# Optimization experiments

Measured on AMD Instinct MI355X. Metric: run time of the kernel, lower is better.

## Reference

```python
import jax, jax.numpy as jnp
import numpy as np

ANG = 7
N = ANG * ANG          # 49 views
CENTER = N // 2        # index 24 = central view
EDGE_C = 150.0
ALPHA = 0.1
CROP = 8
GAUSS = jnp.array([[0.0751, 0.1238, 0.0751],
                   [0.1238, 0.2042, 0.1238],
                   [0.0751, 0.1238, 0.0751]], dtype=jnp.float32)


def _edge_aware_smoothness(D, I):
    # D: [b,h,w] disparity; I: [b,3,h,w] center view
    gx = I[:, :, :, 1:] - I[:, :, :, :-1]
    gy = I[:, :, 1:, :] - I[:, :, :-1, :]
    wx = jnp.exp(-EDGE_C * jnp.mean(jnp.abs(gx), axis=1, keepdims=True))
    wy = jnp.exp(-EDGE_C * jnp.mean(jnp.abs(gy), axis=1, keepdims=True))
    Du = D[:, None]
    dgx = Du[:, :, :, 1:] - Du[:, :, :, :-1]
    dgy = Du[:, :, 1:, :] - Du[:, :, :-1, :]
    lx = jnp.mean((wx * jnp.abs(dgx))[:, :, CROP:-CROP, CROP:-CROP])
    ly = jnp.mean((wy * jnp.abs(dgy))[:, :, CROP:-CROP, CROP:-CROP])
    return (lx + ly) / 2.0


def _warp_all(pred, x):
    # Backward-warp each of the 49 views toward the center view using the
    # per-pixel disparity scaled by the view's angular offset (bilinear,
    # border-clamped) -- standard light-field warping (warp_all in the repo).
    # pred: [b,h,w]; x: [b,3,N,h,w] -> warped [b,3,N,h,w]
    b, c, n, h, w = x.shape
    off = jnp.arange(ANG, dtype=pred.dtype) - (ANG // 2)
    du = jnp.repeat(off, ANG)   # row (u) offset per view, [N]
    dv = jnp.tile(off, ANG)     # col (v) offset per view, [N]
    gy = jnp.arange(h, dtype=pred.dtype)[:, None]
    gx = jnp.arange(w, dtype=pred.dtype)[None, :]
    p = pred[:, None, :, :]                                # [b,1,h,w]
    cy = jnp.clip(gy[None, None] + p * du[None, :, None, None], 0.0, h - 1)
    cx = jnp.clip(gx[None, None] + p * dv[None, :, None, None], 0.0, w - 1)
    y0f = jnp.floor(cy); x0f = jnp.floor(cx)
    ty = (cy - y0f)[..., None]; tx = (cx - x0f)[..., None]
    y0 = y0f.astype(jnp.int32); x0 = x0f.astype(jnp.int32)
    y1 = jnp.minimum(y0 + 1, h - 1); x1 = jnp.minimum(x0 + 1, w - 1)
    img = jnp.transpose(x, (0, 2, 3, 4, 1)).reshape(b, n, h * w, c)

    def gather(yi, xi):
        idx = (yi * w + xi).reshape(b, n, h * w, 1)
        return jnp.take_along_axis(img, idx, axis=2).reshape(b, n, h, w, c)

    out = (gather(y0, x0) * (1 - ty) * (1 - tx)
           + gather(y0, x1) * (1 - ty) * tx
           + gather(y1, x0) * ty * (1 - tx)
           + gather(y1, x1) * ty * tx)
    return jnp.transpose(out, (0, 4, 1, 2, 3))


def _gauss_smooth_angular(cl):
    # cl [b,1,N,h,w]: 3x3 gaussian conv over the 7x7 angular grid, replicate pad
    b, _, _, h, w = cl.shape
    g = cl.reshape(b, 1, ANG, ANG, h, w)
    g = jnp.pad(g, ((0, 0), (0, 0), (1, 1), (1, 1), (0, 0), (0, 0)), mode='edge')
    out = sum(GAUSS[i, j] * g[:, :, i:i + ANG, j:j + ANG]
              for i in range(3) for j in range(3))
    return out.reshape(b, 1, N, h, w)


def _forward(pred, x, y, epoch):
    b, u, v, h, w, c = x.shape
    # 'b u v h w c -> b c (u v) h w'
    xr = jnp.transpose(x, (0, 5, 1, 2, 3, 4)).reshape(b, c, N, h, w)
    center = xr[:, :, CENTER]                               # [b,3,h,w]
    grad_loss = _edge_aware_smoothness(pred, center)
    warped = _warp_all(pred, xr)                            # [b,3,N,h,w]
    color_loss = jnp.mean(jnp.abs(warped - warped[:, :, CENTER:CENTER + 1]),
                          axis=1, keepdims=True)            # [b,1,N,h,w]
    if epoch > 0:
        gauss = jax.lax.stop_gradient(_gauss_smooth_angular(color_loss))
        idx = jnp.argsort(-gauss, axis=2)                   # descending
        sorted_cl = jnp.take_along_axis(color_loss, idx, axis=2)
    else:
        sorted_cl = -jnp.sort(-color_loss, axis=2)
    yb = y[:, None, None, :, :]
    ar = jnp.arange(N, dtype=y.dtype)[None, None, :, None, None]
    mask = (ar > yb).astype(color_loss.dtype) / (N - yb) * N
    if epoch > 0:
        mask = jax.lax.stop_gradient(mask)                  # torch no_grad branch
    cl = jnp.mean((sorted_cl * mask)[..., CROP:-CROP, CROP:-CROP])
    return cl + grad_loss * ALPHA


def setup_inputs():
    key = jax.random.key(0)
    k1, k2, k3 = jax.random.split(key, 3)
    b, h, w = 4, 256, 256
    pred = jax.random.normal(k1, (b, h, w), dtype=jnp.float32)
    x = jax.random.uniform(k2, (b, ANG, ANG, h, w, 3), dtype=jnp.float32)
    y = jax.random.uniform(k3, (b, h, w), dtype=jnp.float32) * 24.0  # keep ~half views
    return {"pred": pred, "x": x, "y": y, "epoch": 5}


def reference(pred, x, y, epoch):
    return _forward(pred, x, y, epoch)
```

## Files before the change

kernel.cpp:

```cpp
#include <hip/hip_runtime.h>
#include <math.h>

#define ANGN 7
#define NV   49
#define CTR  24
#define Himg 256
#define Wimg 256
#define NB   4
#define CROPV 8
#define RW   240
#define RWH  (RW*RW)
#define NPIX (NB*RWH)

__global__ __launch_bounds__(256) void grad_kernel(
    const float* __restrict__ pred, const float* __restrict__ x,
    double* __restrict__ acc)
{
    int eid = blockIdx.x * 256 + threadIdx.x;
    int b   = eid / RWH;
    int rem = eid - b * RWH;
    int ry  = rem / RW;
    int yy  = CROPV + ry;
    int xx  = CROPV + (rem - ry * RW);

    const float* I  = x + (((b * 7 + 3) * 7 + 3) * Himg * Wimg) * 3;
    const float* pr = pred + b * Himg * Wimg;
    int pidx = yy * Wimg + xx;
    const float* q = I + pidx * 3;
    float a0 = q[0], a1 = q[1], a2 = q[2];

    float lx = 0.0f, ly = 0.0f;
    if (xx <= 246) {
        float g0 = fabsf(q[3] - a0), g1 = fabsf(q[4] - a1), g2 = fabsf(q[5] - a2);
        float wx = expf(-150.0f * ((g0 + g1 + g2) * (1.0f / 3.0f)));
        lx = wx * fabsf(pr[pidx + 1] - pr[pidx]);
    }
    if (yy <= 246) {
        const float* r = q + Wimg * 3;
        float g0 = fabsf(r[0] - a0), g1 = fabsf(r[1] - a1), g2 = fabsf(r[2] - a2);
        float wy = expf(-150.0f * ((g0 + g1 + g2) * (1.0f / 3.0f)));
        ly = wy * fabsf(pr[pidx + Wimg] - pr[pidx]);
    }

    #pragma unroll
    for (int off = 32; off > 0; off >>= 1) {
        lx += __shfl_down(lx, off);
        ly += __shfl_down(ly, off);
    }
    __shared__ float sred[8];
    int lane = threadIdx.x & 63, wid = threadIdx.x >> 6;
    if (lane == 0) { sred[wid] = lx; sred[4 + wid] = ly; }
    __syncthreads();
    if (threadIdx.x == 0) {
        atomicAdd(acc + 1, (double)(sred[0] + sred[1] + sred[2] + sred[3]));
        atomicAdd(acc + 2, (double)(sred[4] + sred[5] + sred[6] + sred[7]));
    }
}

__global__ __launch_bounds__(256) void color_kernel(
    const float* __restrict__ pred, const float* __restrict__ x,
    const float* __restrict__ y, const int* __restrict__ epoch_p,
    double* __restrict__ acc)
{
    __shared__ float s_cl[64 * NV];
    __shared__ float s_g [64 * NV];
    __shared__ float sred[4];

    const int tid = threadIdx.x;
    const int pix = tid & 63;
    const int sub = tid >> 6;

    int pid = blockIdx.x * 64 + pix;
    int b   = pid / RWH;
    int rem = pid - b * RWH;
    int ry  = rem / RW;
    int yy  = CROPV + ry;
    int xx  = CROPV + (rem - ry * RW);

    int pidx = (b * Himg + yy) * Wimg + xx;
    float p = pred[pidx];

    const float* cbase = x + ((((b * 7 + 3) * 7 + 3) * Himg + yy) * Wimg + xx) * 3;
    float c0 = cbase[0], c1 = cbase[1], c2 = cbase[2];

    float* mycl = s_cl + pix * NV;
    float* myg  = s_g  + pix * NV;

    for (int n = sub; n < NV; n += 4) {
        int u = n / 7;
        int v = n - u * 7;
        float du = (float)(u - 3), dv = (float)(v - 3);
        float cy = fminf(fmaxf((float)yy + p * du, 0.0f), 255.0f);
        float cx = fminf(fmaxf((float)xx + p * dv, 0.0f), 255.0f);
        float y0f = floorf(cy), x0f = floorf(cx);
        float ty = cy - y0f,   tx = cx - x0f;
        int iy0 = (int)y0f,    ix0 = (int)x0f;
        int iy1 = min(iy0 + 1, 255), ix1 = min(ix0 + 1, 255);

        const float* vb  = x + (((b * 7 + u) * 7 + v) * Himg * Wimg) * 3;
        const float* r0  = vb + iy0 * (Wimg * 3);
        const float* r1  = vb + iy1 * (Wimg * 3);
        const float* p00 = r0 + ix0 * 3;
        const float* p01 = r0 + ix1 * 3;
        const float* p10 = r1 + ix0 * 3;
        const float* p11 = r1 + ix1 * 3;

        float w00 = (1.0f - ty) * (1.0f - tx);
        float w01 = (1.0f - ty) * tx;
        float w10 = ty * (1.0f - tx);
        float w11 = ty * tx;

        float o0 = p00[0] * w00 + p01[0] * w01 + p10[0] * w10 + p11[0] * w11;
        float o1 = p00[1] * w00 + p01[1] * w01 + p10[1] * w10 + p11[1] * w11;
        float o2 = p00[2] * w00 + p01[2] * w01 + p10[2] * w10 + p11[2] * w11;

        mycl[n] = (fabsf(o0 - c0) + fabsf(o1 - c1) + fabsf(o2 - c2)) * (1.0f / 3.0f);
    }
    __syncthreads();

    int epoch = *epoch_p;

    if (epoch > 0) {
        const float gw[9] = {0.0751f, 0.1238f, 0.0751f,
                             0.1238f, 0.2042f, 0.1238f,
                             0.0751f, 0.1238f, 0.0751f};
        for (int n = sub; n < NV; n += 4) {
            int u = n / 7;
            int v = n - u * 7;
            float s = 0.0f;
            #pragma unroll
            for (int i = 0; i < 3; i++) {
                int uu = min(max(u + i - 1, 0), 6);
                #pragma unroll
                for (int j = 0; j < 3; j++) {
                    int vv = min(max(v + j - 1, 0), 6);
                    s += gw[i * 3 + j] * mycl[uu * 7 + vv];
                }
            }
            myg[n] = s;
        }
    }
    __syncthreads();

    const float* key = (epoch > 0) ? myg : mycl;
    float yval = y[pidx];

    float gn[13];
    int   cnt[13];
    #pragma unroll
    for (int i = 0; i < 13; i++) {
        int n = sub + 4 * i;
        gn[i] = (n < NV) ? key[n] : 0.0f;
        cnt[i] = 0;
    }
    for (int m = 0; m < NV; m++) {
        float gm = key[m];
        #pragma unroll
        for (int i = 0; i < 13; i++) {
            int n = sub + 4 * i;
            if (n < NV) {
                cnt[i] += (gm > gn[i]) ? 1 : 0;
                if (m < n) cnt[i] += (gm == gn[i]) ? 1 : 0;
            }
        }
    }
    float tail = 0.0f;
    #pragma unroll
    for (int i = 0; i < 13; i++) {
        int n = sub + 4 * i;
        if (n < NV) {
            tail += ((float)cnt[i] > yval) ? mycl[n] : 0.0f;
        }
    }
    float contrib = tail * (49.0f / (49.0f - yval));

    #pragma unroll
    for (int off = 32; off > 0; off >>= 1)
        contrib += __shfl_down(contrib, off);
    int lane = tid & 63, wid = tid >> 6;
    if (lane == 0) sred[wid] = contrib;
    __syncthreads();
    if (tid == 0)
        atomicAdd(acc + 0, (double)(sred[0] + sred[1] + sred[2] + sred[3]));
}

__global__ void finalize_kernel(const double* __restrict__ acc,
                                float* __restrict__ out)
{
    double cl = acc[0] / 11289600.0;
    double gl = (acc[1] + acc[2]) / (2.0 * 229440.0);
    out[0] = (float)(cl + 0.1 * gl);
}

extern "C" void kernel_launch(void* const* d_in, const int* in_sizes, int n_in,
                              void* d_out, int out_size, void* d_ws, size_t ws_size,
                              hipStream_t stream)
{
    const float* pred  = (const float*)d_in[0];
    const float* x     = (const float*)d_in[1];
    const float* y     = (const float*)d_in[2];
    const int*   epoch = (const int*)d_in[3];
    double* acc = (double*)d_ws;

    hipMemsetAsync(acc, 0, 3 * sizeof(double), stream);
    grad_kernel<<<NPIX / 256, 256, 0, stream>>>(pred, x, acc);
    color_kernel<<<NPIX / 64, 256, 0, stream>>>(pred, x, y, epoch, acc);
    finalize_kernel<<<1, 1, 0, stream>>>(acc, (float*)d_out);
}
```

Measured before the change: 352.1 us.

## Fuse smoothness into color kernel, hoist column coords, pack sort keys

Folds the edge-aware smoothness computation into the color kernel's fourth warp group, so the separate grad kernel launch goes away. Column offsets and weights are precomputed per view column and reused across the seven rows. Each row view is processed with two 24-byte contiguous loads and separable lerps. The rank computation packs the float key bits with the view index into a 64-bit key, so tie-breaking becomes a single comparison. Block indices are swizzled across groups of 8, and the smoothing uses fully unrolled macros; the work split across the four warps is uneven (warp 3 does one row plus the grad terms).

```diff
diff --git a/kernel.cpp b/kernel.cpp
--- a/kernel.cpp
+++ b/kernel.cpp
@@ -1,61 +1,55 @@
 #include <hip/hip_runtime.h>
 #include <math.h>
 
-#define ANGN 7
-#define NV   49
-#define CTR  24
-#define Himg 256
-#define Wimg 256
-#define NB   4
-#define CROPV 8
-#define RW   240
-#define RWH  (RW*RW)
-#define NPIX (NB*RWH)
+#define NV    49
+#define Himg  256
+#define Wimg  256
+#define RW    240
+#define RWH   (RW*RW)
+#define NPIX  (4*RWH)
+#define ROWF  (Wimg*3)
+#define IMGF  (Himg*Wimg*3)
+#define NBLK  (NPIX/64)
 
-__global__ __launch_bounds__(256) void grad_kernel(
-    const float* __restrict__ pred, const float* __restrict__ x,
-    double* __restrict__ acc)
-{
-    int eid = blockIdx.x * 256 + threadIdx.x;
-    int b   = eid / RWH;
-    int rem = eid - b * RWH;
-    int ry  = rem / RW;
-    int yy  = CROPV + ry;
-    int xx  = CROPV + (rem - ry * RW);
 
-    const float* I  = x + (((b * 7 + 3) * 7 + 3) * Himg * Wimg) * 3;
-    const float* pr = pred + b * Himg * Wimg;
-    int pidx = yy * Wimg + xx;
-    const float* q = I + pidx * 3;
-    float a0 = q[0], a1 = q[1], a2 = q[2];
+#define CL7(a) ((a)<0?0:((a)>6?6:(a)))
 
-    float lx = 0.0f, ly = 0.0f;
-    if (xx <= 246) {
-        float g0 = fabsf(q[3] - a0), g1 = fabsf(q[4] - a1), g2 = fabsf(q[5] - a2);
-        float wx = expf(-150.0f * ((g0 + g1 + g2) * (1.0f / 3.0f)));
-        lx = wx * fabsf(pr[pidx + 1] - pr[pidx]);
-    }
-    if (yy <= 246) {
-        const float* r = q + Wimg * 3;
-        float g0 = fabsf(r[0] - a0), g1 = fabsf(r[1] - a1), g2 = fabsf(r[2] - a2);
-        float wy = expf(-150.0f * ((g0 + g1 + g2) * (1.0f / 3.0f)));
-        ly = wy * fabsf(pr[pidx + Wimg] - pr[pidx]);
-    }
+#define DO_VIEW(UC, VC) { \
+    const float* s0p = xv + ((UC)*7 + (VC)) * IMGF + ro0 + co[VC]; \
+    const float* s1p = xv + ((UC)*7 + (VC)) * IMGF + ro1 + co[VC]; \
+    float s0[6], s1[6]; \
+    __builtin_memcpy(s0, s0p, 24); \
+    __builtin_memcpy(s1, s1p, 24); \
+    float tx = txv[VC]; \
+    float h0 = s0[0] + tx*(s0[3]-s0[0]); \
+    float h1 = s0[1] + tx*(s0[4]-s0[1]); \
+    float h2 = s0[2] + tx*(s0[5]-s0[2]); \
+    float k0 = s1[0] + tx*(s1[3]-s1[0]); \
+    float k1 = s1[1] + tx*(s1[4]-s1[1]); \
+    float k2 = s1[2] + tx*(s1[5]-s1[2]); \
+    float o0 = h0 + ty*(k0-h0); \
+    float o1 = h1 + ty*(k1-h1); \
+    float o2 = h2 + ty*(k2-h2); \
+    mycl[(UC)*7+(VC)] = (fabsf(o0-c0)+fabsf(o1-c1)+fabsf(o2-c2)) * (1.0f/3.0f); \
+}
 
-    #pragma unroll
-    for (int off = 32; off > 0; off >>= 1) {
-        lx += __shfl_down(lx, off);
-        ly += __shfl_down(ly, off);
-    }
-    __shared__ float sred[8];
-    int lane = threadIdx.x & 63, wid = threadIdx.x >> 6;
-    if (lane == 0) { sred[wid] = lx; sred[4 + wid] = ly; }
-    __syncthreads();
-    if (threadIdx.x == 0) {
-        atomicAdd(acc + 1, (double)(sred[0] + sred[1] + sred[2] + sred[3]));
-        atomicAdd(acc + 2, (double)(sred[4] + sred[5] + sred[6] + sred[7]));
-    }
+#define DO_U(UC) { \
+    float cy = fminf(fmaxf((float)yy + p * (float)((UC)-3), 0.0f), 255.0f); \
+    float y0f = floorf(cy); \
+    float ty = cy - y0f; \
+    int iy0 = (int)y0f; \
+    int iy1 = min(iy0+1, 255); \
+    int ro0 = iy0*ROWF, ro1 = iy1*ROWF; \
+    DO_VIEW(UC,0) DO_VIEW(UC,1) DO_VIEW(UC,2) DO_VIEW(UC,3) \
+    DO_VIEW(UC,4) DO_VIEW(UC,5) DO_VIEW(UC,6) \
 }
+
+#define GV(UC,VC) myg[(UC)*7+(VC)] = \
+    0.0751f*mycl[CL7((UC)-1)*7+CL7((VC)-1)] + 0.1238f*mycl[CL7((UC)-1)*7+(VC)] + 0.0751f*mycl[CL7((UC)-1)*7+CL7((VC)+1)] + \
+    0.1238f*mycl[(UC)*7+CL7((VC)-1)]        + 0.2042f*mycl[(UC)*7+(VC)]        + 0.1238f*mycl[(UC)*7+CL7((VC)+1)] + \
+    0.0751f*mycl[CL7((UC)+1)*7+CL7((VC)-1)] + 0.1238f*mycl[CL7((UC)+1)*7+(VC)] + 0.0751f*mycl[CL7((UC)+1)*7+CL7((VC)+1)];
+
+#define GU(UC) GV(UC,0) GV(UC,1) GV(UC,2) GV(UC,3) GV(UC,4) GV(UC,5) GV(UC,6)
 
 __global__ __launch_bounds__(256) void color_kernel(
     const float* __restrict__ pred, const float* __restrict__ x,
@@ -70,115 +64,107 @@
     const int pix = tid & 63;
     const int sub = tid >> 6;
 
-    int pid = blockIdx.x * 64 + pix;
+    int lb  = (blockIdx.x & 7) * (NBLK/8) + (blockIdx.x >> 3);
+    int pid = lb * 64 + pix;
     int b   = pid / RWH;
     int rem = pid - b * RWH;
     int ry  = rem / RW;
-    int yy  = CROPV + ry;
-    int xx  = CROPV + (rem - ry * RW);
+    int yy  = 8 + ry;
+    int xx  = 8 + (rem - ry * RW);
 
     int pidx = (b * Himg + yy) * Wimg + xx;
     float p = pred[pidx];
 
-    const float* cbase = x + ((((b * 7 + 3) * 7 + 3) * Himg + yy) * Wimg + xx) * 3;
+    const float* xv    = x + (size_t)b * (49 * IMGF);
+    const float* cbase = xv + (24 * IMGF) + (yy * Wimg + xx) * 3;
     float c0 = cbase[0], c1 = cbase[1], c2 = cbase[2];
 
     float* mycl = s_cl + pix * NV;
     float* myg  = s_g  + pix * NV;
 
-    for (int n = sub; n < NV; n += 4) {
-        int u = n / 7;
-        int v = n - u * 7;
-        float du = (float)(u - 3), dv = (float)(v - 3);
-        float cy = fminf(fmaxf((float)yy + p * du, 0.0f), 255.0f);
-        float cx = fminf(fmaxf((float)xx + p * dv, 0.0f), 255.0f);
-        float y0f = floorf(cy), x0f = floorf(cx);
-        float ty = cy - y0f,   tx = cx - x0f;
-        int iy0 = (int)y0f,    ix0 = (int)x0f;
-        int iy1 = min(iy0 + 1, 255), ix1 = min(ix0 + 1, 255);
+    int co[7]; float txv[7];
+    #pragma unroll
+    for (int vv = 0; vv < 7; vv++) {
+        float cx = fminf(fmaxf((float)xx + p * (float)(vv-3), 0.0f), 255.0f);
+        float x0f = floorf(cx);
+        float tx = cx - x0f;
+        int ix0 = (int)x0f;
+        if (ix0 >= 255) { ix0 = 254; tx = 1.0f; }
+        co[vv] = ix0 * 3; txv[vv] = tx;
+    }
 
-        const float* vb  = x + (((b * 7 + u) * 7 + v) * Himg * Wimg) * 3;
-        const float* r0  = vb + iy0 * (Wimg * 3);
-        const float* r1  = vb + iy1 * (Wimg * 3);
-        const float* p00 = r0 + ix0 * 3;
-        const float* p01 = r0 + ix1 * 3;
-        const float* p10 = r1 + ix0 * 3;
-        const float* p11 = r1 + ix1 * 3;
-
-        float w00 = (1.0f - ty) * (1.0f - tx);
-        float w01 = (1.0f - ty) * tx;
-        float w10 = ty * (1.0f - tx);
-        float w11 = ty * tx;
-
-        float o0 = p00[0] * w00 + p01[0] * w01 + p10[0] * w10 + p11[0] * w11;
-        float o1 = p00[1] * w00 + p01[1] * w01 + p10[1] * w10 + p11[1] * w11;
-        float o2 = p00[2] * w00 + p01[2] * w01 + p10[2] * w10 + p11[2] * w11;
-
-        mycl[n] = (fabsf(o0 - c0) + fabsf(o1 - c1) + fabsf(o2 - c2)) * (1.0f / 3.0f);
+    if (sub == 0)      { DO_U(0) DO_U(4) }
+    else if (sub == 1) { DO_U(1) DO_U(5) }
+    else if (sub == 2) { DO_U(2) DO_U(6) }
+    else {
+        DO_U(3)
+        float lx = 0.0f, ly = 0.0f;
+        if (xx <= 246) {
+            float q6[6]; __builtin_memcpy(q6, cbase, 24);
+            float wx = __expf(-50.0f * (fabsf(q6[3]-c0) + fabsf(q6[4]-c1) + fabsf(q6[5]-c2)));
+            lx = wx * fabsf(pred[pidx + 1] - p);
+        }
+        if (yy <= 246) {
+            float r0 = cbase[ROWF], r1 = cbase[ROWF+1], r2 = cbase[ROWF+2];
+            float wy = __expf(-50.0f * (fabsf(r0-c0) + fabsf(r1-c1) + fabsf(r2-c2)));
+            ly = wy * fabsf(pred[pidx + Wimg] - p);
+        }
+        #pragma unroll
+        for (int off = 32; off > 0; off >>= 1) {
+            lx += __shfl_down(lx, off);
+            ly += __shfl_down(ly, off);
+        }
+        if ((tid & 63) == 0) {
+            atomicAdd(acc + 1, (double)lx);
+            atomicAdd(acc + 2, (double)ly);
+        }
     }
     __syncthreads();
 
-    int epoch = *epoch_p;
+    const int epoch = *epoch_p;
 
     if (epoch > 0) {
-        const float gw[9] = {0.0751f, 0.1238f, 0.0751f,
-                             0.1238f, 0.2042f, 0.1238f,
-                             0.0751f, 0.1238f, 0.0751f};
-        for (int n = sub; n < NV; n += 4) {
-            int u = n / 7;
-            int v = n - u * 7;
-            float s = 0.0f;
-            #pragma unroll
-            for (int i = 0; i < 3; i++) {
-                int uu = min(max(u + i - 1, 0), 6);
-                #pragma unroll
-                for (int j = 0; j < 3; j++) {
-                    int vv = min(max(v + j - 1, 0), 6);
-                    s += gw[i * 3 + j] * mycl[uu * 7 + vv];
-                }
-            }
-            myg[n] = s;
-        }
+        if (sub == 0)      { GU(0) GU(4) }
+        else if (sub == 1) { GU(1) GU(5) }
+        else if (sub == 2) { GU(2) GU(6) }
+        else               { GU(3) }
     }
     __syncthreads();
 
     const float* key = (epoch > 0) ? myg : mycl;
     float yval = y[pidx];
 
-    float gn[13];
-    int   cnt[13];
+    unsigned long long kn[13];
+    int cnt[13];
     #pragma unroll
     for (int i = 0; i < 13; i++) {
-        int n = sub + 4 * i;
-        gn[i] = (n < NV) ? key[n] : 0.0f;
+        int n = sub + 4*i;
+        if (n < NV) {
+            unsigned int bb = __float_as_uint(key[n]);
+            kn[i] = (((unsigned long long)bb) << 8) | (unsigned long long)(255 - n);
+        } else kn[i] = ~0ULL;
         cnt[i] = 0;
     }
     for (int m = 0; m < NV; m++) {
-        float gm = key[m];
+        unsigned int bm = __float_as_uint(key[m]);
+        unsigned long long km = (((unsigned long long)bm) << 8) | (unsigned long long)(255 - m);
         #pragma unroll
-        for (int i = 0; i < 13; i++) {
-            int n = sub + 4 * i;
-            if (n < NV) {
-                cnt[i] += (gm > gn[i]) ? 1 : 0;
-                if (m < n) cnt[i] += (gm == gn[i]) ? 1 : 0;
-            }
-        }
+        for (int i = 0; i < 13; i++)
+            cnt[i] += (km > kn[i]) ? 1 : 0;
     }
     float tail = 0.0f;
     #pragma unroll
     for (int i = 0; i < 13; i++) {
-        int n = sub + 4 * i;
-        if (n < NV) {
+        int n = sub + 4*i;
+        if (n < NV)
             tail += ((float)cnt[i] > yval) ? mycl[n] : 0.0f;
-        }
     }
     float contrib = tail * (49.0f / (49.0f - yval));
 
     #pragma unroll
     for (int off = 32; off > 0; off >>= 1)
         contrib += __shfl_down(contrib, off);
-    int lane = tid & 63, wid = tid >> 6;
-    if (lane == 0) sred[wid] = contrib;
+    if ((tid & 63) == 0) sred[sub] = contrib;
     __syncthreads();
     if (tid == 0)
         atomicAdd(acc + 0, (double)(sred[0] + sred[1] + sred[2] + sred[3]));
@@ -203,7 +189,6 @@
     double* acc = (double*)d_ws;
 
     hipMemsetAsync(acc, 0, 3 * sizeof(double), stream);
-    grad_kernel<<<NPIX / 256, 256, 0, stream>>>(pred, x, acc);
-    color_kernel<<<NPIX / 64, 256, 0, stream>>>(pred, x, y, epoch, acc);
+    color_kernel<<<NBLK, 256, 0, stream>>>(pred, x, y, epoch, acc);
     finalize_kernel<<<1, 1, 0, stream>>>(acc, (float*)d_out);
 }
```

Measured after the change: 325.5 us. -7.6%, faster.
